# Performance work log

Hardware: AMD Instinct MI355X
Metric: run time of the kernel (lower is better)

## Reference

```python
import jax, jax.numpy as jnp
import numpy as np

B, L, D, H, NC = 32, 1024, 256, 512, 16


def setup_inputs() -> dict:
    key = jax.random.key(0)
    ks = jax.random.split(key, 8)
    s_in = 1.0 / np.sqrt(D)
    s_h = 1.0 / np.sqrt(H)
    return {
        "x": jax.random.normal(ks[0], (B, L, D), jnp.float32),
        "W0": jax.random.normal(ks[1], (D, 4 * H), jnp.float32) * s_in,
        "b0": jnp.zeros((2 * H,), jnp.float32),
        "W1": jax.random.normal(ks[2], (H, 3 * H), jnp.float32) * s_h,
        "b1": jnp.zeros((2 * H,), jnp.float32),
        "W2": jax.random.normal(ks[3], (H, 3 * H), jnp.float32) * s_h,
        "b2": jnp.zeros((2 * H,), jnp.float32),
        "W3": jax.random.normal(ks[4], (H, 3 * H), jnp.float32) * s_h,
        "b3": jnp.zeros((2 * H,), jnp.float32),
        "Wp": jax.random.normal(ks[5], (H, H), jnp.float32) * s_h,
        "bp": jnp.zeros((H,), jnp.float32),
        "Wc": jax.random.normal(ks[6], (H, NC), jnp.float32) * s_h,
        "bc": jnp.zeros((NC,), jnp.float32),
    }


def _sru_layer(h, W, b, first):
    # h: (B, L, Din); W: (Din, kH); b: (2H,)
    k = 4 if first else 3
    Hh = W.shape[1] // k
    U = jnp.einsum('bld,dk->blk', h, W)  # (B, L, kH)
    if first:
        xt, fpre, rpre, xres = jnp.split(U, 4, axis=-1)
    else:
        xt, fpre, rpre = jnp.split(U, 3, axis=-1)
        xres = h
    bf, br = jnp.split(b, 2)
    f = jax.nn.sigmoid(fpre + bf)  # forget gate (B, L, H)
    r = jax.nn.sigmoid(rpre + br)  # reset/highway gate

    def step(c, inp):
        f_t, x_t = inp
        c = f_t * c + (1.0 - f_t) * x_t
        return c, c

    c0 = jnp.zeros((h.shape[0], Hh), h.dtype)
    _, c_seq = jax.lax.scan(step, c0, (jnp.swapaxes(f, 0, 1), jnp.swapaxes(xt, 0, 1)))
    c_seq = jnp.swapaxes(c_seq, 0, 1)  # (B, L, H)
    out = r * c_seq + (1.0 - r) * xres  # highway output
    return out, c_seq[:, -1, :]


def reference(x, W0, b0, W1, b1, W2, b2, W3, b3, Wp, bp, Wc, bc):
    h = x
    finals = []
    for W, b, first in ((W0, b0, True), (W1, b1, False), (W2, b2, False), (W3, b3, False)):
        h, cT = _sru_layer(h, W, b, first)
        finals.append(cT)
    hidden = jnp.stack(finals)  # (num_layers, B, H)
    projected = h[:, -1, :] @ Wp + bp
    output = projected @ Wc + bc
    return output, h, hidden
```

## Files before the change

kernel.cpp:

```cpp
#include <hip/hip_runtime.h>

#define DEV_INLINE __device__ __forceinline__

typedef __attribute__((ext_vector_type(8))) short bf16x8;
typedef __attribute__((ext_vector_type(4))) float f32x4;

DEV_INLINE unsigned short f2bf(float f) {
  union { float f; unsigned u; } v; v.f = f;
  unsigned r = v.u + 0x7FFFu + ((v.u >> 16) & 1u);
  return (unsigned short)(r >> 16);
}
DEV_INLINE float bf2f(unsigned short u) {
  union { unsigned u; float f; } v; v.u = ((unsigned)u) << 16;
  return v.f;
}
DEV_INLINE float sigmoidf_(float x) { return 1.0f / (1.0f + __expf(-x)); }

DEV_INLINE void gload_lds16(const void* g, void* l) {
  __builtin_amdgcn_global_load_lds(
      (const __attribute__((address_space(1))) void*)(g),
      (__attribute__((address_space(3))) void*)(l), 16, 0, 0);
}

__global__ __launch_bounds__(256)
void prep_kernel(const float* __restrict__ x, unsigned short* __restrict__ xbf,
                 const float* __restrict__ W0, unsigned short* __restrict__ Wt0,
                 const float* __restrict__ W1, unsigned short* __restrict__ Wt1,
                 const float* __restrict__ W2, unsigned short* __restrict__ Wt2,
                 const float* __restrict__ W3, unsigned short* __restrict__ Wt3) {
  __shared__ float tile[32][33];
  const int id = blockIdx.x;
  const int t = threadIdx.x;
  if (id < 8192) {
    const int i = id * 256 + t;
    const float4 v = reinterpret_cast<const float4*>(x)[i];
    ushort4 o;
    o.x = f2bf(v.x); o.y = f2bf(v.y); o.z = f2bf(v.z); o.w = f2bf(v.w);
    reinterpret_cast<ushort4*>(xbf)[i] = o;
    return;
  }
  int rid = id - 8192;
  const float* W; unsigned short* Wt; int K, N, bx, by;
  if (rid < 512) {
    W = W0; Wt = Wt0; K = 256; N = 2048; bx = rid & 7; by = rid >> 3;
  } else {
    rid -= 512;
    const int seg = rid / 768; rid -= seg * 768;
    K = 512; N = 1536;
    W  = seg == 0 ? W1  : (seg == 1 ? W2  : W3);
    Wt = seg == 0 ? Wt1 : (seg == 1 ? Wt2 : Wt3);
    bx = rid & 15; by = rid >> 4;
  }
  const int tx = t & 31, ty = t >> 5;
  const int kb = bx * 32, nb = by * 32;
  #pragma unroll
  for (int i = 0; i < 32; i += 8)
    tile[ty + i][tx] = W[(size_t)(kb + ty + i) * N + (nb + tx)];
  __syncthreads();
  #pragma unroll
  for (int i = 0; i < 32; i += 8)
    Wt[(size_t)(nb + ty + i) * K + (kb + tx)] = f2bf(tile[tx][ty + i]);
}

__global__ __launch_bounds__(256, 2)
void gemm_gate_kernel(const unsigned short* __restrict__ A,
                      const unsigned short* __restrict__ Bt,
                      const float* __restrict__ bias,
                      unsigned short* __restrict__ U,
                      int N, int K, int NTN) {
  __shared__ short smem[256 * 64 + 128 * 64];
  short* As = smem;
  short* Bs = smem + 256 * 64;

  const int tid = threadIdx.x;
  const int lane = tid & 63;
  const int l15 = lane & 15;
  const int l4 = lane >> 4;
  const int w = tid >> 6;
  const int wrow = (w >> 1) * 128;
  const int wcol = (w & 1) * 64;

  const int nwg = gridDim.x;
  const int cpx = nwg >> 3;
  const int swz = (blockIdx.x & 7) * cpx + (blockIdx.x >> 3);
  const int mtile = swz / NTN;
  const int ntile = swz - mtile * NTN;
  const int m0 = mtile * 256;
  const int n0 = ntile * 128;

  f32x4 acc[8][4];
  #pragma unroll
  for (int i = 0; i < 8; ++i)
    #pragma unroll
    for (int j = 0; j < 4; ++j)
      acc[i][j] = (f32x4){0.f, 0.f, 0.f, 0.f};

  const unsigned short* Abase = A + (size_t)m0 * K;
  const unsigned short* Bbase = Bt + (size_t)n0 * K;
  const int nsteps = K >> 6;

  for (int t = 0; t < nsteps; ++t) {
    const int k0 = t * 64;
    #pragma unroll
    for (int it = 0; it < 8; ++it) {
      int c = it * 256 + tid;
      int row = c >> 3, sl = c & 7;
      int ks = sl ^ (row & 7);
      gload_lds16(Abase + (size_t)row * K + (k0 + ks * 8), &As[c * 8]);
    }
    #pragma unroll
    for (int it = 0; it < 4; ++it) {
      int c = it * 256 + tid;
      int row = c >> 3, sl = c & 7;
      int ks = sl ^ (row & 7);
      gload_lds16(Bbase + (size_t)row * K + (k0 + ks * 8), &Bs[c * 8]);
    }
    __syncthreads();

    const bf16x8* As8 = (const bf16x8*)As;
    const bf16x8* Bs8 = (const bf16x8*)Bs;
    #pragma unroll
    for (int kk = 0; kk < 2; ++kk) {
      bf16x8 af[8], bfr[4];
      #pragma unroll
      for (int i = 0; i < 8; ++i) {
        int r = wrow + i * 16 + l15;
        int phys = (kk * 4 + l4) ^ (r & 7);
        af[i] = As8[r * 8 + phys];
      }
      #pragma unroll
      for (int j = 0; j < 4; ++j) {
        int r = wcol + j * 16 + l15;
        int phys = (kk * 4 + l4) ^ (r & 7);
        bfr[j] = Bs8[r * 8 + phys];
      }
      #pragma unroll
      for (int i = 0; i < 8; ++i)
        #pragma unroll
        for (int j = 0; j < 4; ++j)
          acc[i][j] = __builtin_amdgcn_mfma_f32_16x16x32_bf16(af[i], bfr[j], acc[i][j], 0, 0, 0);
    }
    __syncthreads();
  }

  #pragma unroll
  for (int i = 0; i < 8; ++i) {
    const int grow0 = m0 + wrow + i * 16 + l4 * 4;
    #pragma unroll
    for (int j = 0; j < 4; ++j) {
      const int gcol = n0 + wcol + j * 16 + l15;
      const int region = gcol >> 9;
      const bool gate = (region == 1) | (region == 2);
      const float bval = (region == 1) ? bias[gcol & 511]
                       : ((region == 2) ? bias[512 + (gcol & 511)] : 0.f);
      #pragma unroll
      for (int reg = 0; reg < 4; ++reg) {
        float v = acc[i][j][reg];
        if (gate) v = sigmoidf_(v + bval);
        U[(size_t)(grow0 + reg) * N + gcol] = f2bf(v);
      }
    }
  }
}

__global__ __launch_bounds__(512)
void scan_kernel(const unsigned short* __restrict__ U, int N, int first,
                 const unsigned short* __restrict__ hin,
                 unsigned short* __restrict__ hout_bf,
                 float* __restrict__ hout_f32,
                 float* __restrict__ hidden) {
  const int b = blockIdx.x >> 3;
  const int hslice = blockIdx.x & 7;
  const int hv = threadIdx.x & 7;
  const int ch = threadIdx.x >> 3;
  const int h0 = (hslice << 6) + (hv << 3);
  __shared__ float sP[64 * 68];
  __shared__ float sQ[64 * 68];

  const size_t rowBase = (size_t)b * 1024 + (size_t)ch * 16;
  const unsigned short* Uxt = U + rowBase * N + h0;

  float c[8], P[8];
  #pragma unroll
  for (int j = 0; j < 8; ++j) { c[j] = 0.f; P[j] = 1.f; }
  {
    const unsigned short* px = Uxt;
    const unsigned short* pf = Uxt + 512;
    #pragma unroll 2
    for (int l = 0; l < 16; ++l) {
      bf16x8 xv = *(const bf16x8*)px;
      bf16x8 fv = *(const bf16x8*)pf;
      #pragma unroll
      for (int j = 0; j < 8; ++j) {
        float f  = bf2f((unsigned short)fv[j]);
        float xt = bf2f((unsigned short)xv[j]);
        c[j] = f * c[j] + (1.f - f) * xt;
        P[j] *= f;
      }
      px += N; pf += N;
    }
  }
  float* myP = &sP[ch * 68 + hv * 8];
  float* myQ = &sQ[ch * 68 + hv * 8];
  #pragma unroll
  for (int j = 0; j < 8; ++j) { myP[j] = P[j]; myQ[j] = c[j]; }
  __syncthreads();

  for (int s = 1; s < 64; s <<= 1) {
    const int src = (ch >= s) ? (ch - s) : ch;
    float pp[8], pq[8];
    const float* qP = &sP[src * 68 + hv * 8];
    const float* qQ = &sQ[src * 68 + hv * 8];
    #pragma unroll
    for (int j = 0; j < 8; ++j) { pp[j] = qP[j]; pq[j] = qQ[j]; }
    asm volatile("s_waitcnt lgkmcnt(0)" ::: "memory");
    __builtin_amdgcn_sched_barrier(0);
    __syncthreads();
    if (ch >= s) {
      #pragma unroll
      for (int j = 0; j < 8; ++j) {
        c[j] = P[j] * pq[j] + c[j];
        P[j] = P[j] * pp[j];
        myP[j] = P[j]; myQ[j] = c[j];
      }
    }
    __syncthreads();
  }

  float cc[8];
  if (ch == 0) {
    #pragma unroll
    for (int j = 0; j < 8; ++j) cc[j] = 0.f;
  } else {
    const float* qQ = &sQ[(ch - 1) * 68 + hv * 8];
    #pragma unroll
    for (int j = 0; j < 8; ++j) cc[j] = qQ[j];
  }

  const unsigned short* px = Uxt;
  const unsigned short* pf = Uxt + 512;
  const unsigned short* pr = Uxt + 1024;
  const unsigned short* pxr = first ? (Uxt + 1536) : (hin + rowBase * 512 + h0);
  const int xr_stride = first ? N : 512;
  unsigned short* ob = hout_bf ? hout_bf + rowBase * 512 + h0 : (unsigned short*)nullptr;
  float* of = hout_f32 ? hout_f32 + rowBase * 512 + h0 : (float*)nullptr;
  #pragma unroll 2
  for (int l = 0; l < 16; ++l) {
    bf16x8 xv = *(const bf16x8*)px;
    bf16x8 fv = *(const bf16x8*)pf;
    bf16x8 rv = *(const bf16x8*)pr;
    bf16x8 xrv = *(const bf16x8*)pxr;
    bf16x8 obuf;
    float ofl[8];
    #pragma unroll
    for (int j = 0; j < 8; ++j) {
      float f  = bf2f((unsigned short)fv[j]);
      float xt = bf2f((unsigned short)xv[j]);
      cc[j] = f * cc[j] + (1.f - f) * xt;
      float r  = bf2f((unsigned short)rv[j]);
      float xr = bf2f((unsigned short)xrv[j]);
      float o = r * cc[j] + (1.f - r) * xr;
      obuf[j] = (short)f2bf(o);
      ofl[j] = o;
    }
    if (ob) { *(bf16x8*)ob = obuf; ob += 512; }
    if (of) {
      *(float4*)of = make_float4(ofl[0], ofl[1], ofl[2], ofl[3]);
      *(float4*)(of + 4) = make_float4(ofl[4], ofl[5], ofl[6], ofl[7]);
      of += 512;
    }
    px += N; pf += N; pr += N; pxr += xr_stride;
  }
  if (ch == 63) {
    #pragma unroll
    for (int j = 0; j < 8; ++j) hidden[(size_t)b * 512 + h0 + j] = cc[j];
  }
}

__global__ __launch_bounds__(256)
void proj_kernel(const float* __restrict__ hfull, const float* __restrict__ Wp,
                 const float* __restrict__ bp, const float* __restrict__ Wc,
                 const float* __restrict__ bc, float* __restrict__ out) {
  __shared__ float hl[512];
  __shared__ float pr[512];
  const int b = blockIdx.x, t = threadIdx.x;
  const float* hrow = hfull + ((size_t)b * 1024 + 1023) * 512;
  hl[t] = hrow[t];
  hl[t + 256] = hrow[t + 256];
  __syncthreads();
  for (int j = t; j < 512; j += 256) {
    float s = 0.f;
    for (int k = 0; k < 512; ++k) s += hl[k] * Wp[(size_t)k * 512 + j];
    pr[j] = s + bp[j];
  }
  __syncthreads();
  if (t < 16) {
    float s = 0.f;
    for (int k = 0; k < 512; ++k) s += pr[k] * Wc[k * 16 + t];
    out[b * 16 + t] = s + bc[t];
  }
}

extern "C" void kernel_launch(void* const* d_in, const int* in_sizes, int n_in,
                              void* d_out, int out_size, void* d_ws, size_t ws_size,
                              hipStream_t stream) {
  const float* x  = (const float*)d_in[0];
  const float* W0 = (const float*)d_in[1];
  const float* b0 = (const float*)d_in[2];
  const float* W1 = (const float*)d_in[3];
  const float* b1 = (const float*)d_in[4];
  const float* W2 = (const float*)d_in[5];
  const float* b2 = (const float*)d_in[6];
  const float* W3 = (const float*)d_in[7];
  const float* b3 = (const float*)d_in[8];
  const float* Wp = (const float*)d_in[9];
  const float* bp = (const float*)d_in[10];
  const float* Wc = (const float*)d_in[11];
  const float* bc = (const float*)d_in[12];

  float* out = (float*)d_out;
  float* outO = out;
  float* outH = out + 512;
  float* outHid = out + 512 + (size_t)32 * 1024 * 512;

  char* ws = (char*)d_ws;
  size_t off = 0;
  auto alloc = [&](size_t bytes) {
    void* p = ws + off;
    off += (bytes + 255) & ~(size_t)255;
    return p;
  };
  unsigned short* Wt0 = (unsigned short*)alloc((size_t)2048 * 256 * 2);
  unsigned short* Wt1 = (unsigned short*)alloc((size_t)1536 * 512 * 2);
  unsigned short* Wt2 = (unsigned short*)alloc((size_t)1536 * 512 * 2);
  unsigned short* Wt3 = (unsigned short*)alloc((size_t)1536 * 512 * 2);
  unsigned short* xbf = (unsigned short*)alloc((size_t)32768 * 256 * 2);
  unsigned short* h0  = (unsigned short*)alloc((size_t)32768 * 512 * 2);
  unsigned short* h1  = (unsigned short*)alloc((size_t)32768 * 512 * 2);
  unsigned short* Ubf = (unsigned short*)alloc((size_t)32768 * 2048 * 2);
  (void)ws_size; (void)in_sizes; (void)n_in; (void)out_size;

  prep_kernel<<<8192 + 512 + 3 * 768, 256, 0, stream>>>(
      x, xbf, W0, Wt0, W1, Wt1, W2, Wt2, W3, Wt3);

  gemm_gate_kernel<<<128 * 16, 256, 0, stream>>>(xbf, Wt0, b0, Ubf, 2048, 256, 16);
  scan_kernel<<<256, 512, 0, stream>>>(Ubf, 2048, 1, nullptr, h0, nullptr, outHid + 0);
  gemm_gate_kernel<<<128 * 12, 256, 0, stream>>>(h0, Wt1, b1, Ubf, 1536, 512, 12);
  scan_kernel<<<256, 512, 0, stream>>>(Ubf, 1536, 0, h0, h1, nullptr, outHid + 16384);
  gemm_gate_kernel<<<128 * 12, 256, 0, stream>>>(h1, Wt2, b2, Ubf, 1536, 512, 12);
  scan_kernel<<<256, 512, 0, stream>>>(Ubf, 1536, 0, h1, h0, nullptr, outHid + 32768);
  gemm_gate_kernel<<<128 * 12, 256, 0, stream>>>(h0, Wt3, b3, Ubf, 1536, 512, 12);
  scan_kernel<<<256, 512, 0, stream>>>(Ubf, 1536, 0, h0, nullptr, outH, outHid + 49152);

  proj_kernel<<<32, 256, 0, stream>>>(outH, Wp, bp, Wc, bc, outO);
}
```

Before: 569.5 us.

## Replace LDS-staged GEMM with direct global fragment loads and smaller tiles

The gate GEMM no longer stages A and B tiles through shared memory with global_load_lds and barriers. Each wave now loads its MFMA fragments straight from global memory into registers. The block tile shrinks from 256x128 to 128x128, doubling the grid, and launch bounds rise to 4 blocks per SIMD for higher occupancy. This drops the LDS round trip and the syncthreads, but loses cross-wave reuse, so each A/B row is fetched by several waves and L2 traffic rises.

```diff
diff --git a/kernel.cpp b/kernel.cpp
--- a/kernel.cpp
+++ b/kernel.cpp
@@ -15,12 +15,6 @@
   return v.f;
 }
 DEV_INLINE float sigmoidf_(float x) { return 1.0f / (1.0f + __expf(-x)); }
-
-DEV_INLINE void gload_lds16(const void* g, void* l) {
-  __builtin_amdgcn_global_load_lds(
-      (const __attribute__((address_space(1))) void*)(g),
-      (__attribute__((address_space(3))) void*)(l), 16, 0, 0);
-}
 
 __global__ __launch_bounds__(256)
 void prep_kernel(const float* __restrict__ x, unsigned short* __restrict__ xbf,
@@ -62,93 +56,73 @@
     Wt[(size_t)(nb + ty + i) * K + (kb + tx)] = f2bf(tile[tx][ty + i]);
 }
 
-__global__ __launch_bounds__(256, 2)
+__global__ __launch_bounds__(256, 4)
 void gemm_gate_kernel(const unsigned short* __restrict__ A,
                       const unsigned short* __restrict__ Bt,
                       const float* __restrict__ bias,
                       unsigned short* __restrict__ U,
                       int N, int K, int NTN) {
-  __shared__ short smem[256 * 64 + 128 * 64];
-  short* As = smem;
-  short* Bs = smem + 256 * 64;
-
   const int tid = threadIdx.x;
   const int lane = tid & 63;
   const int l15 = lane & 15;
   const int l4 = lane >> 4;
   const int w = tid >> 6;
-  const int wrow = (w >> 1) * 128;
-  const int wcol = (w & 1) * 64;
+  const int wr = (w >> 1) * 64;
+  const int wc = (w & 1) * 64;
 
   const int nwg = gridDim.x;
   const int cpx = nwg >> 3;
   const int swz = (blockIdx.x & 7) * cpx + (blockIdx.x >> 3);
   const int mtile = swz / NTN;
   const int ntile = swz - mtile * NTN;
-  const int m0 = mtile * 256;
+  const int m0 = mtile * 128;
   const int n0 = ntile * 128;
 
-  f32x4 acc[8][4];
-  #pragma unroll
-  for (int i = 0; i < 8; ++i)
+  f32x4 acc[4][4];
+  #pragma unroll
+  for (int i = 0; i < 4; ++i)
     #pragma unroll
     for (int j = 0; j < 4; ++j)
       acc[i][j] = (f32x4){0.f, 0.f, 0.f, 0.f};
 
-  const unsigned short* Abase = A + (size_t)m0 * K;
-  const unsigned short* Bbase = Bt + (size_t)n0 * K;
+  const unsigned short* pA[4];
+  const unsigned short* pB[4];
+  #pragma unroll
+  for (int i = 0; i < 4; ++i) {
+    pA[i] = A  + (size_t)(m0 + wr + i * 16 + l15) * K + l4 * 8;
+    pB[i] = Bt + (size_t)(n0 + wc + i * 16 + l15) * K + l4 * 8;
+  }
+
   const int nsteps = K >> 6;
-
   for (int t = 0; t < nsteps; ++t) {
-    const int k0 = t * 64;
-    #pragma unroll
-    for (int it = 0; it < 8; ++it) {
-      int c = it * 256 + tid;
-      int row = c >> 3, sl = c & 7;
-      int ks = sl ^ (row & 7);
-      gload_lds16(Abase + (size_t)row * K + (k0 + ks * 8), &As[c * 8]);
-    }
-    #pragma unroll
-    for (int it = 0; it < 4; ++it) {
-      int c = it * 256 + tid;
-      int row = c >> 3, sl = c & 7;
-      int ks = sl ^ (row & 7);
-      gload_lds16(Bbase + (size_t)row * K + (k0 + ks * 8), &Bs[c * 8]);
-    }
-    __syncthreads();
-
-    const bf16x8* As8 = (const bf16x8*)As;
-    const bf16x8* Bs8 = (const bf16x8*)Bs;
-    #pragma unroll
-    for (int kk = 0; kk < 2; ++kk) {
-      bf16x8 af[8], bfr[4];
-      #pragma unroll
-      for (int i = 0; i < 8; ++i) {
-        int r = wrow + i * 16 + l15;
-        int phys = (kk * 4 + l4) ^ (r & 7);
-        af[i] = As8[r * 8 + phys];
-      }
-      #pragma unroll
-      for (int j = 0; j < 4; ++j) {
-        int r = wcol + j * 16 + l15;
-        int phys = (kk * 4 + l4) ^ (r & 7);
-        bfr[j] = Bs8[r * 8 + phys];
-      }
-      #pragma unroll
-      for (int i = 0; i < 8; ++i)
-        #pragma unroll
-        for (int j = 0; j < 4; ++j)
-          acc[i][j] = __builtin_amdgcn_mfma_f32_16x16x32_bf16(af[i], bfr[j], acc[i][j], 0, 0, 0);
-    }
-    __syncthreads();
-  }
-
-  #pragma unroll
-  for (int i = 0; i < 8; ++i) {
-    const int grow0 = m0 + wrow + i * 16 + l4 * 4;
+    bf16x8 a0[4], a1[4], b0[4], b1[4];
+    #pragma unroll
+    for (int i = 0; i < 4; ++i) {
+      a0[i] = *(const bf16x8*)(pA[i]);
+      a1[i] = *(const bf16x8*)(pA[i] + 32);
+      b0[i] = *(const bf16x8*)(pB[i]);
+      b1[i] = *(const bf16x8*)(pB[i] + 32);
+    }
+    #pragma unroll
+    for (int i = 0; i < 4; ++i)
+      #pragma unroll
+      for (int j = 0; j < 4; ++j)
+        acc[i][j] = __builtin_amdgcn_mfma_f32_16x16x32_bf16(a0[i], b0[j], acc[i][j], 0, 0, 0);
+    #pragma unroll
+    for (int i = 0; i < 4; ++i)
+      #pragma unroll
+      for (int j = 0; j < 4; ++j)
+        acc[i][j] = __builtin_amdgcn_mfma_f32_16x16x32_bf16(a1[i], b1[j], acc[i][j], 0, 0, 0);
+    #pragma unroll
+    for (int i = 0; i < 4; ++i) { pA[i] += 64; pB[i] += 64; }
+  }
+
+  #pragma unroll
+  for (int i = 0; i < 4; ++i) {
+    const int grow0 = m0 + wr + i * 16 + l4 * 4;
     #pragma unroll
     for (int j = 0; j < 4; ++j) {
-      const int gcol = n0 + wcol + j * 16 + l15;
+      const int gcol = n0 + wc + j * 16 + l15;
       const int region = gcol >> 9;
       const bool gate = (region == 1) | (region == 2);
       const float bval = (region == 1) ? bias[gcol & 511]
@@ -343,13 +317,13 @@
   prep_kernel<<<8192 + 512 + 3 * 768, 256, 0, stream>>>(
       x, xbf, W0, Wt0, W1, Wt1, W2, Wt2, W3, Wt3);
 
-  gemm_gate_kernel<<<128 * 16, 256, 0, stream>>>(xbf, Wt0, b0, Ubf, 2048, 256, 16);
+  gemm_gate_kernel<<<256 * 16, 256, 0, stream>>>(xbf, Wt0, b0, Ubf, 2048, 256, 16);
   scan_kernel<<<256, 512, 0, stream>>>(Ubf, 2048, 1, nullptr, h0, nullptr, outHid + 0);
-  gemm_gate_kernel<<<128 * 12, 256, 0, stream>>>(h0, Wt1, b1, Ubf, 1536, 512, 12);
+  gemm_gate_kernel<<<256 * 12, 256, 0, stream>>>(h0, Wt1, b1, Ubf, 1536, 512, 12);
   scan_kernel<<<256, 512, 0, stream>>>(Ubf, 1536, 0, h0, h1, nullptr, outHid + 16384);
-  gemm_gate_kernel<<<128 * 12, 256, 0, stream>>>(h1, Wt2, b2, Ubf, 1536, 512, 12);
+  gemm_gate_kernel<<<256 * 12, 256, 0, stream>>>(h1, Wt2, b2, Ubf, 1536, 512, 12);
   scan_kernel<<<256, 512, 0, stream>>>(Ubf, 1536, 0, h1, h0, nullptr, outHid + 32768);
-  gemm_gate_kernel<<<128 * 12, 256, 0, stream>>>(h0, Wt3, b3, Ubf, 1536, 512, 12);
+  gemm_gate_kernel<<<256 * 12, 256, 0, stream>>>(h0, Wt3, b3, Ubf, 1536, 512, 12);
   scan_kernel<<<256, 512, 0, stream>>>(Ubf, 1536, 0, h0, nullptr, outH, outHid + 49152);
 
   proj_kernel<<<32, 256, 0, stream>>>(outH, Wp, bp, Wc, bc, outO);
```

Measured after the change: 947.4 us. 66.3% more time.
